# Performance work log

Hardware: AMD Instinct MI355X
Metric: run time of the kernel (lower is better)

The kernel has to match this reference:

```python
import jax, jax.numpy as jnp
import numpy as np

N = 50000   # nodes
E = 800000  # edges (avg degree 16)
D = 128     # in_dim == out_dim
EPS = 1e-5  # LayerNorm eps (torch default)


def setup_inputs() -> dict:
    key = jax.random.key(0)
    ks = jax.random.split(key, 8)
    x = jax.random.normal(ks[0], (N, D), dtype=jnp.float32)
    edge_row = jax.random.randint(ks[1], (E,), 0, N, dtype=jnp.int32)
    edge_col = jax.random.randint(ks[2], (E,), 0, N, dtype=jnp.int32)
    edge_val = jax.random.uniform(ks[3], (E,), dtype=jnp.float32)
    W = jax.random.normal(ks[4], (D, D), dtype=jnp.float32) / np.sqrt(D).astype(np.float32)
    b = jnp.zeros((D,), jnp.float32)
    gamma = jnp.ones((D,), jnp.float32)
    beta = jnp.zeros((D,), jnp.float32)
    return {"x": x, "edge_val": edge_val, "W": W, "b": b,
            "gamma": gamma, "beta": beta,
            "edge_row": edge_row, "edge_col": edge_col}


def reference(x, edge_val, W, b, gamma, beta, edge_row, edge_col):
    # SpMM: support = adj @ x, adj in COO form (row, col, val)
    msgs = edge_val[:, None] * x[edge_col]                      # [E, D] gather
    support = jax.ops.segment_sum(msgs, edge_row, num_segments=x.shape[0])  # [N, D]
    # Linear (torch stores weight as [out, in])
    h = support @ W.T + b                                       # [N, D]
    # LayerNorm over last dim
    mu = jnp.mean(h, axis=-1, keepdims=True)
    var = jnp.mean(jnp.square(h - mu), axis=-1, keepdims=True)
    h = (h - mu) * jax.lax.rsqrt(var + EPS) * gamma + beta
    # ReLU; dropout is identity at inference
    return jax.nn.relu(h)
```

## Files before the change

### kernel.cpp

```cpp
#include <hip/hip_runtime.h>

#define D 128
#define LN_EPS 1e-5f
#define RPB 16
#define POISON 0xAAAAAAAAu
#define ECAP 68
#define EMAX 64
#define KBB 256
#define KBT 1024
#define DCAP 3200
#define NFB 4096
#define XST_STRIDE 68
#define GT_PER 4

typedef __attribute__((ext_vector_type(8))) short short8;
typedef __attribute__((ext_vector_type(4))) float f32x4;

union FragU { uint4 u; short8 s; };

__device__ __forceinline__ unsigned bf16_hi(float f) {
    unsigned u = __float_as_uint(f);
    return (u + 0x7FFFu + ((u >> 16) & 1u)) & 0xFFFF0000u;
}
__device__ __forceinline__ float lo16f(unsigned u) { return __uint_as_float(u << 16); }
__device__ __forceinline__ float hi16f(unsigned u) { return __uint_as_float(u & 0xFFFF0000u); }

__global__ void __launch_bounds__(KBT) bin_kernel(
    const int* __restrict__ edge_row, const int* __restrict__ edge_col,
    const float* __restrict__ edge_val, const float* __restrict__ W,
    unsigned* __restrict__ Wb, uint2* __restrict__ binbuf,
    int* __restrict__ tab, int E, int epb) {
    __shared__ uint2 dense[DCAP];
    __shared__ int cnt[NFB];
    __shared__ int tmp[2][KBT];
    int t = threadIdx.x;
    int blk = blockIdx.x;

    if (blk == 0) {
        for (int i = t; i < 8192; i += KBT) {
            int u  = i & 3;
            int L  = (i >> 2) & 63;
            int nt = (i >> 8) & 7;
            int kt = i >> 11;
            int n = nt * 16 + (L & 15);
            int k = kt * 32 + (L >> 4) * 8 + u * 2;
            Wb[i] = bf16_hi(W[n * D + k + 1]) | (bf16_hi(W[n * D + k]) >> 16);
        }
    }

    for (int i = t; i < NFB; i += KBT) cnt[i] = 0;
    __syncthreads();

    int e0 = blk * epb;
    int e1 = e0 + epb; if (e1 > E) e1 = E;
    int nume = e1 - e0; if (nume < 0) nume = 0;
    int quadEnd = e0 + (nume & ~3);

    for (int i = e0 + t * 4; i + 3 < quadEnd + 4 && i + 3 < e1; i += KBT * 4) {
        int4 r = *(const int4*)(edge_row + i);
        atomicAdd(&cnt[r.x >> 4], 1);
        atomicAdd(&cnt[r.y >> 4], 1);
        atomicAdd(&cnt[r.z >> 4], 1);
        atomicAdd(&cnt[r.w >> 4], 1);
    }
    for (int i = quadEnd + t; i < e1; i += KBT) atomicAdd(&cnt[edge_row[i] >> 4], 1);
    __syncthreads();

    {
        int i0 = t * 4;
        int a0 = cnt[i0], a1 = cnt[i0 + 1], a2 = cnt[i0 + 2], a3 = cnt[i0 + 3];
        int s1 = a0 + a1, s2 = s1 + a2, tot = s2 + a3;
        tmp[0][t] = tot;
        __syncthreads();
        int buf = 0;
        for (int off = 1; off < KBT; off <<= 1) {
            int v = tmp[buf][t];
            if (t >= off) v += tmp[buf][t - off];
            tmp[1 - buf][t] = v;
            buf ^= 1;
            __syncthreads();
        }
        int base = tmp[buf][t] - tot;
        cnt[i0] = base; cnt[i0 + 1] = base + a0;
        cnt[i0 + 2] = base + s1; cnt[i0 + 3] = base + s2;
    }
    __syncthreads();

    for (int i = t; i < NFB; i += KBT) tab[blk * NFB + i] = cnt[i];
    __syncthreads();

    for (int i = e0 + t * 4; i + 3 < e1; i += KBT * 4) {
        int4 r = *(const int4*)(edge_row + i);
        int4 c = *(const int4*)(edge_col + i);
        float4 v = *(const float4*)(edge_val + i);
        int p0 = atomicAdd(&cnt[r.x >> 4], 1);
        int p1 = atomicAdd(&cnt[r.y >> 4], 1);
        int p2 = atomicAdd(&cnt[r.z >> 4], 1);
        int p3 = atomicAdd(&cnt[r.w >> 4], 1);
        dense[p0] = make_uint2(((unsigned)c.x << 16) | (unsigned)(r.x & 15), bf16_hi(v.x));
        dense[p1] = make_uint2(((unsigned)c.y << 16) | (unsigned)(r.y & 15), bf16_hi(v.y));
        dense[p2] = make_uint2(((unsigned)c.z << 16) | (unsigned)(r.z & 15), bf16_hi(v.z));
        dense[p3] = make_uint2(((unsigned)c.w << 16) | (unsigned)(r.w & 15), bf16_hi(v.w));
    }
    for (int i = quadEnd + t; i < e1; i += KBT) {
        int r = edge_row[i];
        int p = atomicAdd(&cnt[r >> 4], 1);
        dense[p] = make_uint2(((unsigned)edge_col[i] << 16) | (unsigned)(r & 15),
                              bf16_hi(edge_val[i]));
    }
    __syncthreads();

    for (int i = t; i < nume; i += KBT)
        binbuf[(size_t)blk * DCAP + i] = dense[i];
}

__global__ void __launch_bounds__(256) gemm_kernel(
    const float* __restrict__ x, const unsigned* __restrict__ Wb,
    unsigned* __restrict__ yb16, int N) {
    __shared__ unsigned xst[RPB][XST_STRIDE];
    int t = threadIdx.x;
    int T = (N + RPB - 1) / RPB;
    for (int it = 0; it < GT_PER; ++it) {
        int tile = (int)blockIdx.x * GT_PER + it;
        if (tile >= T) break;
        {
            int r = t >> 4, q = t & 15;
            int row = tile * RPB + r;
            uint4 o = make_uint4(0u, 0u, 0u, 0u);
            if (row < N) {
                float4 a = *(const float4*)(x + (size_t)row * D + q * 8);
                float4 c = *(const float4*)(x + (size_t)row * D + q * 8 + 4);
                o.x = bf16_hi(a.y) | (bf16_hi(a.x) >> 16);
                o.y = bf16_hi(a.w) | (bf16_hi(a.z) >> 16);
                o.z = bf16_hi(c.y) | (bf16_hi(c.x) >> 16);
                o.w = bf16_hi(c.w) | (bf16_hi(c.z) >> 16);
            }
            *(uint4*)&xst[r][q * 4] = o;
        }
        __syncthreads();
        {
            int L = t & 63;
            int w = t >> 6;
            int m = L & 15;
            int gk = L >> 4;
            f32x4 acc0 = {0.f, 0.f, 0.f, 0.f};
            f32x4 acc1 = {0.f, 0.f, 0.f, 0.f};
#pragma unroll
            for (int kt = 0; kt < 4; ++kt) {
                FragU a, b0, b1;
                a.u  = *(const uint4*)&xst[m][kt * 16 + gk * 4];
                b0.u = *(const uint4*)(Wb + (((size_t)(kt * 8 + w * 2)) * 64 + L) * 4);
                b1.u = *(const uint4*)(Wb + (((size_t)(kt * 8 + w * 2 + 1)) * 64 + L) * 4);
                acc0 = __builtin_amdgcn_mfma_f32_16x16x32_bf16(a.s, b0.s, acc0, 0, 0, 0);
                acc1 = __builtin_amdgcn_mfma_f32_16x16x32_bf16(a.s, b1.s, acc1, 0, 0, 0);
            }
            bool evenm = (m & 1) == 0;
#pragma unroll
            for (int i = 0; i < 4; ++i) {
                float p0 = __shfl_xor(acc0[i], 1);
                float p1 = __shfl_xor(acc1[i], 1);
                if (evenm) {
                    int row = tile * RPB + gk * 4 + i;
                    if (row < N) {
                        unsigned y0 = bf16_hi(p0) | (bf16_hi(acc0[i]) >> 16);
                        unsigned y1 = bf16_hi(p1) | (bf16_hi(acc1[i]) >> 16);
                        size_t base = (size_t)row * (D / 2) + w * 16 + (m >> 1);
                        yb16[base] = y0;
                        yb16[base + 8] = y1;
                    }
                }
            }
        }
        __syncthreads();
    }
}

__global__ void __launch_bounds__(256) fused_lite(
    const unsigned* __restrict__ yb16, const uint2* __restrict__ binbuf,
    const int* __restrict__ tab,
    const float* __restrict__ bias, const float* __restrict__ gamma,
    const float* __restrict__ beta, float* __restrict__ out, int N) {
    __shared__ unsigned ecol[RPB][ECAP];
    __shared__ int ecnt[RPB];
    __shared__ int pdeg[RPB];
    int t = threadIdx.x;
    int f = blockIdx.x;
    int row0 = f * RPB;

    if (t < RPB) ecnt[t] = 0;
    int s = tab[t * NFB + f];
    int e = tab[t * NFB + f + 1];
    __syncthreads();

    {
        const uint2* bp = binbuf + (size_t)t * DCAP;
        for (int idx = s; idx < e; ++idx) {
            uint2 rec = bp[idx];
            int rl = (int)(rec.x & 15u);
            int p = atomicAdd(&ecnt[rl], 1);
            if (p < EMAX) ecol[rl][p] = rec.y | (rec.x >> 16);
        }
    }
    __syncthreads();
    if (t < RPB) {
        int c = ecnt[t]; if (c > EMAX) c = EMAX;
        int pe = (c + 3) & ~3;
        for (int k = c; k < pe; ++k) ecol[t][k] = 0;
        pdeg[t] = pe;
    }
    __syncthreads();

    {
        int r = t >> 4;
        int qd = t & 15;
        int row = row0 + r;
        float4 accA = make_float4(0.f, 0.f, 0.f, 0.f);
        float4 accB = make_float4(0.f, 0.f, 0.f, 0.f);
        if (row < N) {
            int pd = pdeg[r];
            const unsigned* yb = yb16 + qd * 4;
            for (int e4 = 0; e4 < pd; e4 += 4) {
                uint4 p = *(const uint4*)&ecol[r][e4];
                unsigned c0 = p.x & 0xFFFFu, c1 = p.y & 0xFFFFu;
                unsigned c2 = p.z & 0xFFFFu, c3 = p.w & 0xFFFFu;
                float w0 = __uint_as_float(p.x & 0xFFFF0000u);
                float w1 = __uint_as_float(p.y & 0xFFFF0000u);
                float w2 = __uint_as_float(p.z & 0xFFFF0000u);
                float w3 = __uint_as_float(p.w & 0xFFFF0000u);
                uint4 X0 = *(const uint4*)(yb + (size_t)c0 * (D / 2));
                uint4 X1 = *(const uint4*)(yb + (size_t)c1 * (D / 2));
                uint4 X2 = *(const uint4*)(yb + (size_t)c2 * (D / 2));
                uint4 X3 = *(const uint4*)(yb + (size_t)c3 * (D / 2));
                accA.x = fmaf(w0, lo16f(X0.x), accA.x);
                accA.y = fmaf(w0, hi16f(X0.x), accA.y);
                accA.z = fmaf(w0, lo16f(X0.y), accA.z);
                accA.w = fmaf(w0, hi16f(X0.y), accA.w);
                accB.x = fmaf(w0, lo16f(X0.z), accB.x);
                accB.y = fmaf(w0, hi16f(X0.z), accB.y);
                accB.z = fmaf(w0, lo16f(X0.w), accB.z);
                accB.w = fmaf(w0, hi16f(X0.w), accB.w);
                accA.x = fmaf(w1, lo16f(X1.x), accA.x);
                accA.y = fmaf(w1, hi16f(X1.x), accA.y);
                accA.z = fmaf(w1, lo16f(X1.y), accA.z);
                accA.w = fmaf(w1, hi16f(X1.y), accA.w);
                accB.x = fmaf(w1, lo16f(X1.z), accB.x);
                accB.y = fmaf(w1, hi16f(X1.z), accB.y);
                accB.z = fmaf(w1, lo16f(X1.w), accB.z);
                accB.w = fmaf(w1, hi16f(X1.w), accB.w);
                accA.x = fmaf(w2, lo16f(X2.x), accA.x);
                accA.y = fmaf(w2, hi16f(X2.x), accA.y);
                accA.z = fmaf(w2, lo16f(X2.y), accA.z);
                accA.w = fmaf(w2, hi16f(X2.y), accA.w);
                accB.x = fmaf(w2, lo16f(X2.z), accB.x);
                accB.y = fmaf(w2, hi16f(X2.z), accB.y);
                accB.z = fmaf(w2, lo16f(X2.w), accB.z);
                accB.w = fmaf(w2, hi16f(X2.w), accB.w);
                accA.x = fmaf(w3, lo16f(X3.x), accA.x);
                accA.y = fmaf(w3, hi16f(X3.x), accA.y);
                accA.z = fmaf(w3, lo16f(X3.y), accA.z);
                accA.w = fmaf(w3, hi16f(X3.y), accA.w);
                accB.x = fmaf(w3, lo16f(X3.z), accB.x);
                accB.y = fmaf(w3, hi16f(X3.z), accB.y);
                accB.z = fmaf(w3, lo16f(X3.w), accB.z);
                accB.w = fmaf(w3, hi16f(X3.w), accB.w);
            }
        }
        float4 bA = *(const float4*)(bias + qd * 8);
        float4 bB = *(const float4*)(bias + qd * 8 + 4);
        accA.x += bA.x; accA.y += bA.y; accA.z += bA.z; accA.w += bA.w;
        accB.x += bB.x; accB.y += bB.y; accB.z += bB.z; accB.w += bB.w;

        float sum = accA.x + accA.y + accA.z + accA.w
                  + accB.x + accB.y + accB.z + accB.w;
        float sq = accA.x * accA.x;
        sq = fmaf(accA.y, accA.y, sq);
        sq = fmaf(accA.z, accA.z, sq);
        sq = fmaf(accA.w, accA.w, sq);
        sq = fmaf(accB.x, accB.x, sq);
        sq = fmaf(accB.y, accB.y, sq);
        sq = fmaf(accB.z, accB.z, sq);
        sq = fmaf(accB.w, accB.w, sq);
#pragma unroll
        for (int off = 8; off > 0; off >>= 1) {
            sum += __shfl_xor(sum, off, 16);
            sq  += __shfl_xor(sq, off, 16);
        }
        float mu = sum * (1.0f / D);
        float var = sq * (1.0f / D) - mu * mu;
        float inv = rsqrtf(var + LN_EPS);

        if (row < N) {
            float4 gA = *(const float4*)(gamma + qd * 8);
            float4 gB = *(const float4*)(gamma + qd * 8 + 4);
            float4 eA = *(const float4*)(beta + qd * 8);
            float4 eB = *(const float4*)(beta + qd * 8 + 4);
            float4 oA, oB;
            oA.x = fmaxf((accA.x - mu) * inv * gA.x + eA.x, 0.f);
            oA.y = fmaxf((accA.y - mu) * inv * gA.y + eA.y, 0.f);
            oA.z = fmaxf((accA.z - mu) * inv * gA.z + eA.z, 0.f);
            oA.w = fmaxf((accA.w - mu) * inv * gA.w + eA.w, 0.f);
            oB.x = fmaxf((accB.x - mu) * inv * gB.x + eB.x, 0.f);
            oB.y = fmaxf((accB.y - mu) * inv * gB.y + eB.y, 0.f);
            oB.z = fmaxf((accB.z - mu) * inv * gB.z + eB.z, 0.f);
            oB.w = fmaxf((accB.w - mu) * inv * gB.w + eB.w, 0.f);
            *(float4*)(out + (size_t)row * D + qd * 8) = oA;
            *(float4*)(out + (size_t)row * D + qd * 8 + 4) = oB;
        }
    }
}

extern "C" void kernel_launch(void* const* d_in, const int* in_sizes, int n_in,
                              void* d_out, int out_size, void* d_ws, size_t ws_size,
                              hipStream_t stream) {
    const float* x        = (const float*)d_in[0];
    const float* edge_val = (const float*)d_in[1];
    const float* W        = (const float*)d_in[2];
    const float* b        = (const float*)d_in[3];
    const float* gamma    = (const float*)d_in[4];
    const float* beta     = (const float*)d_in[5];
    const int*   edge_row = (const int*)d_in[6];
    const int*   edge_col = (const int*)d_in[7];

    const int N = in_sizes[0] / D;
    const int E = in_sizes[1];
    const int T = (N + RPB - 1) / RPB;

    char* ws = (char*)d_ws;
    uint2*    binbuf = (uint2*)ws;    ws += (size_t)KBB * DCAP * sizeof(uint2);
    int*      tab    = (int*)ws;      ws += (size_t)KBB * NFB * sizeof(int);
    unsigned* yb16   = (unsigned*)ws; ws += (size_t)N * (D / 2) * sizeof(unsigned);
    unsigned* Wb     = (unsigned*)ws; ws += 8192 * sizeof(unsigned);

    int epb = ((E + KBB - 1) / KBB + 3) & ~3;

    bin_kernel<<<KBB, KBT, 0, stream>>>(edge_row, edge_col, edge_val, W,
                                        Wb, binbuf, tab, E, epb);
    gemm_kernel<<<(T + GT_PER - 1) / GT_PER, 256, 0, stream>>>(x, Wb, yb16, N);
    fused_lite<<<T, 256, 0, stream>>>(yb16, binbuf, tab, b, gamma, beta,
                                      (float*)d_out, N);
}
```

Measured before the change: 141.1 us.

## Fuse edge binning and x@W GEMM into one prep kernel; remap fused blocks per XCD

Merges the binning kernel and the bf16 MFMA GEMM kernel into a single prep kernel. Each block converts W into the MFMA fragment layout in its own LDS, reusing the binning arena, and then runs the GEMM over a grid-strided set of tiles, four tiles at a time across its 1024 threads. This removes a kernel launch and the global Wb round trip. In exchange, every block redundantly builds the W fragments, and the GEMM is limited to 256 blocks that hold a 50 KB LDS arena. The fused kernel's block index is also remapped so that consecutive row tiles land on the same XCD, aimed at L2 locality.

After: 135.3 us, median of 2. 4.1% less time.

```diff
diff --git a/kernel.cpp b/kernel.cpp
--- a/kernel.cpp
+++ b/kernel.cpp
@@ -11,7 +11,6 @@
 #define DCAP 3200
 #define NFB 4096
 #define XST_STRIDE 68
-#define GT_PER 4
 
 typedef __attribute__((ext_vector_type(8))) short short8;
 typedef __attribute__((ext_vector_type(4))) float f32x4;
@@ -25,28 +24,21 @@
 __device__ __forceinline__ float lo16f(unsigned u) { return __uint_as_float(u << 16); }
 __device__ __forceinline__ float hi16f(unsigned u) { return __uint_as_float(u & 0xFFFF0000u); }
 
-__global__ void __launch_bounds__(KBT) bin_kernel(
+__global__ void __launch_bounds__(KBT) prep_kernel(
     const int* __restrict__ edge_row, const int* __restrict__ edge_col,
     const float* __restrict__ edge_val, const float* __restrict__ W,
-    unsigned* __restrict__ Wb, uint2* __restrict__ binbuf,
-    int* __restrict__ tab, int E, int epb) {
-    __shared__ uint2 dense[DCAP];
-    __shared__ int cnt[NFB];
-    __shared__ int tmp[2][KBT];
+    const float* __restrict__ x, unsigned* __restrict__ yb16,
+    uint2* __restrict__ binbuf, int* __restrict__ tab,
+    int E, int N, int epb) {
+    __shared__ __align__(16) char arena[50176];
+    uint2* dense = (uint2*)arena;
+    int*   cnt   = (int*)(arena + 25600);
+    int (*tmp)[KBT] = (int(*)[KBT])(arena + 41984);
+    unsigned* wbL = (unsigned*)arena;
+    typedef unsigned XstRow[XST_STRIDE];
+    XstRow* xstA = (XstRow*)(arena + 32768);
     int t = threadIdx.x;
     int blk = blockIdx.x;
-
-    if (blk == 0) {
-        for (int i = t; i < 8192; i += KBT) {
-            int u  = i & 3;
-            int L  = (i >> 2) & 63;
-            int nt = (i >> 8) & 7;
-            int kt = i >> 11;
-            int n = nt * 16 + (L & 15);
-            int k = kt * 32 + (L >> 4) * 8 + u * 2;
-            Wb[i] = bf16_hi(W[n * D + k + 1]) | (bf16_hi(W[n * D + k]) >> 16);
-        }
-    }
 
     for (int i = t; i < NFB; i += KBT) cnt[i] = 0;
     __syncthreads();
@@ -56,7 +48,7 @@
     int nume = e1 - e0; if (nume < 0) nume = 0;
     int quadEnd = e0 + (nume & ~3);
 
-    for (int i = e0 + t * 4; i + 3 < quadEnd + 4 && i + 3 < e1; i += KBT * 4) {
+    for (int i = e0 + t * 4; i + 3 < e1; i += KBT * 4) {
         int4 r = *(const int4*)(edge_row + i);
         atomicAdd(&cnt[r.x >> 4], 1);
         atomicAdd(&cnt[r.y >> 4], 1);
@@ -112,66 +104,76 @@
 
     for (int i = t; i < nume; i += KBT)
         binbuf[(size_t)blk * DCAP + i] = dense[i];
-}
-
-__global__ void __launch_bounds__(256) gemm_kernel(
-    const float* __restrict__ x, const unsigned* __restrict__ Wb,
-    unsigned* __restrict__ yb16, int N) {
-    __shared__ unsigned xst[RPB][XST_STRIDE];
-    int t = threadIdx.x;
-    int T = (N + RPB - 1) / RPB;
-    for (int it = 0; it < GT_PER; ++it) {
-        int tile = (int)blockIdx.x * GT_PER + it;
-        if (tile >= T) break;
-        {
-            int r = t >> 4, q = t & 15;
-            int row = tile * RPB + r;
-            uint4 o = make_uint4(0u, 0u, 0u, 0u);
-            if (row < N) {
-                float4 a = *(const float4*)(x + (size_t)row * D + q * 8);
-                float4 c = *(const float4*)(x + (size_t)row * D + q * 8 + 4);
-                o.x = bf16_hi(a.y) | (bf16_hi(a.x) >> 16);
-                o.y = bf16_hi(a.w) | (bf16_hi(a.z) >> 16);
-                o.z = bf16_hi(c.y) | (bf16_hi(c.x) >> 16);
-                o.w = bf16_hi(c.w) | (bf16_hi(c.z) >> 16);
+    __syncthreads();
+
+    for (int i = t; i < 8192; i += KBT) {
+        int u  = i & 3;
+        int L  = (i >> 2) & 63;
+        int nt = (i >> 8) & 7;
+        int kt = i >> 11;
+        int n = nt * 16 + (L & 15);
+        int k = kt * 32 + (L >> 4) * 8 + u * 2;
+        wbL[i] = bf16_hi(W[n * D + k + 1]) | (bf16_hi(W[n * D + k]) >> 16);
+    }
+    __syncthreads();
+
+    {
+        int T = (N + RPB - 1) / RPB;
+        int g = t >> 8;
+        int tg = t & 255;
+        XstRow* xst = xstA + g * RPB;
+        for (int tb0 = blk * 4; tb0 < T; tb0 += gridDim.x * 4) {
+            int tile = tb0 + g;
+            if (tile < T) {
+                int r = tg >> 4, q = tg & 15;
+                int row = tile * RPB + r;
+                uint4 o = make_uint4(0u, 0u, 0u, 0u);
+                if (row < N) {
+                    float4 a = *(const float4*)(x + (size_t)row * D + q * 8);
+                    float4 c = *(const float4*)(x + (size_t)row * D + q * 8 + 4);
+                    o.x = bf16_hi(a.y) | (bf16_hi(a.x) >> 16);
+                    o.y = bf16_hi(a.w) | (bf16_hi(a.z) >> 16);
+                    o.z = bf16_hi(c.y) | (bf16_hi(c.x) >> 16);
+                    o.w = bf16_hi(c.w) | (bf16_hi(c.z) >> 16);
+                }
+                *(uint4*)&xst[r][q * 4] = o;
             }
-            *(uint4*)&xst[r][q * 4] = o;
-        }
-        __syncthreads();
-        {
-            int L = t & 63;
-            int w = t >> 6;
-            int m = L & 15;
-            int gk = L >> 4;
-            f32x4 acc0 = {0.f, 0.f, 0.f, 0.f};
-            f32x4 acc1 = {0.f, 0.f, 0.f, 0.f};
+            __syncthreads();
+            if (tile < T) {
+                int L = tg & 63;
+                int w = tg >> 6;
+                int m = L & 15;
+                int gk = L >> 4;
+                f32x4 acc0 = {0.f, 0.f, 0.f, 0.f};
+                f32x4 acc1 = {0.f, 0.f, 0.f, 0.f};
 #pragma unroll
-            for (int kt = 0; kt < 4; ++kt) {
-                FragU a, b0, b1;
-                a.u  = *(const uint4*)&xst[m][kt * 16 + gk * 4];
-                b0.u = *(const uint4*)(Wb + (((size_t)(kt * 8 + w * 2)) * 64 + L) * 4);
-                b1.u = *(const uint4*)(Wb + (((size_t)(kt * 8 + w * 2 + 1)) * 64 + L) * 4);
-                acc0 = __builtin_amdgcn_mfma_f32_16x16x32_bf16(a.s, b0.s, acc0, 0, 0, 0);
-                acc1 = __builtin_amdgcn_mfma_f32_16x16x32_bf16(a.s, b1.s, acc1, 0, 0, 0);
-            }
-            bool evenm = (m & 1) == 0;
+                for (int kt = 0; kt < 4; ++kt) {
+                    FragU a, b0, b1;
+                    a.u  = *(const uint4*)&xst[m][kt * 16 + gk * 4];
+                    b0.u = *(const uint4*)(wbL + (((size_t)(kt * 8 + w * 2)) * 64 + L) * 4);
+                    b1.u = *(const uint4*)(wbL + (((size_t)(kt * 8 + w * 2 + 1)) * 64 + L) * 4);
+                    acc0 = __builtin_amdgcn_mfma_f32_16x16x32_bf16(a.s, b0.s, acc0, 0, 0, 0);
+                    acc1 = __builtin_amdgcn_mfma_f32_16x16x32_bf16(a.s, b1.s, acc1, 0, 0, 0);
+                }
+                bool evenm = (m & 1) == 0;
 #pragma unroll
-            for (int i = 0; i < 4; ++i) {
-                float p0 = __shfl_xor(acc0[i], 1);
-                float p1 = __shfl_xor(acc1[i], 1);
-                if (evenm) {
-                    int row = tile * RPB + gk * 4 + i;
-                    if (row < N) {
-                        unsigned y0 = bf16_hi(p0) | (bf16_hi(acc0[i]) >> 16);
-                        unsigned y1 = bf16_hi(p1) | (bf16_hi(acc1[i]) >> 16);
-                        size_t base = (size_t)row * (D / 2) + w * 16 + (m >> 1);
-                        yb16[base] = y0;
-                        yb16[base + 8] = y1;
+                for (int i = 0; i < 4; ++i) {
+                    float p0 = __shfl_xor(acc0[i], 1);
+                    float p1 = __shfl_xor(acc1[i], 1);
+                    if (evenm) {
+                        int row = tile * RPB + gk * 4 + i;
+                        if (row < N) {
+                            unsigned y0 = bf16_hi(p0) | (bf16_hi(acc0[i]) >> 16);
+                            unsigned y1 = bf16_hi(p1) | (bf16_hi(acc1[i]) >> 16);
+                            size_t base = (size_t)row * (D / 2) + w * 16 + (m >> 1);
+                            yb16[base] = y0;
+                            yb16[base + 8] = y1;
+                        }
                     }
                 }
             }
-        }
-        __syncthreads();
+            __syncthreads();
+        }
     }
 }
 
@@ -184,7 +186,12 @@
     __shared__ int ecnt[RPB];
     __shared__ int pdeg[RPB];
     int t = threadIdx.x;
-    int f = blockIdx.x;
+
+    int nwg = (int)gridDim.x;
+    int swq = nwg >> 3, swr = nwg & 7;
+    int xcd = (int)blockIdx.x & 7;
+    int f = (xcd < swr ? xcd * (swq + 1) : swr * (swq + 1) + (xcd - swr) * swq)
+          + ((int)blockIdx.x >> 3);
     int row0 = f * RPB;
 
     if (t < RPB) ecnt[t] = 0;
@@ -329,13 +336,11 @@
     uint2*    binbuf = (uint2*)ws;    ws += (size_t)KBB * DCAP * sizeof(uint2);
     int*      tab    = (int*)ws;      ws += (size_t)KBB * NFB * sizeof(int);
     unsigned* yb16   = (unsigned*)ws; ws += (size_t)N * (D / 2) * sizeof(unsigned);
-    unsigned* Wb     = (unsigned*)ws; ws += 8192 * sizeof(unsigned);
 
     int epb = ((E + KBB - 1) / KBB + 3) & ~3;
 
-    bin_kernel<<<KBB, KBT, 0, stream>>>(edge_row, edge_col, edge_val, W,
-                                        Wb, binbuf, tab, E, epb);
-    gemm_kernel<<<(T + GT_PER - 1) / GT_PER, 256, 0, stream>>>(x, Wb, yb16, N);
+    prep_kernel<<<KBB, KBT, 0, stream>>>(edge_row, edge_col, edge_val, W, x,
+                                         yb16, binbuf, tab, E, N, epb);
     fused_lite<<<T, 256, 0, stream>>>(yb16, binbuf, tab, b, gamma, beta,
                                       (float*)d_out, N);
 }
```
